# Kernel tuning notes

Hardware: AMD Instinct MI355X
Metric: run time of the kernel (lower is better)

The kernel has to match this reference:

```python
import jax, jax.numpy as jnp
import numpy as np

B, N, C = 4, 2048, 768
H = 12
HD = C // H
SCALE = HD ** -0.5


def setup_inputs() -> dict:
    key = jax.random.key(0)
    k1, k2, k3 = jax.random.split(key, 3)
    x = jax.random.normal(k1, (B, N, C), dtype=jnp.float32)
    w_qkv = jax.random.normal(k2, (3 * C, C), dtype=jnp.float32) * (C ** -0.5)
    w_proj = jax.random.normal(k3, (C, C), dtype=jnp.float32) * (C ** -0.5)
    b_proj = jnp.zeros((C,), dtype=jnp.float32)
    return {"x": x, "w_qkv": w_qkv, "w_proj": w_proj, "b_proj": b_proj}


def reference(x, w_qkv, w_proj, b_proj):
    Bx, Nx, Cx = x.shape
    # qkv linear: x @ W^T -> [B, N, 3C], then split into heads
    qkv = jnp.einsum('bnc,dc->bnd', x, w_qkv)
    qkv = qkv.reshape(Bx, Nx, 3, H, HD).transpose(2, 0, 3, 1, 4)  # [3, B, H, N, HD]
    q, k, v = qkv[0], qkv[1], qkv[2]
    attn = jnp.einsum('bhqd,bhkd->bhqk', q, k) * SCALE  # [B, H, N, N]
    attn = jax.nn.softmax(attn, axis=-1)
    out = jnp.einsum('bhqk,bhkd->bhqd', attn, v)  # [B, H, N, HD]
    out = out.transpose(0, 2, 1, 3).reshape(Bx, Nx, Cx)
    out = jnp.einsum('bnc,dc->bnd', out, w_proj) + b_proj
    return out
```

## Files before the change

### kernel.cpp

```cpp
#include <hip/hip_runtime.h>
#include <hip/hip_bf16.h>
#include <stdint.h>

#define DI __device__ __forceinline__

typedef __bf16 bf16x8 __attribute__((ext_vector_type(8)));
typedef float f32x4 __attribute__((ext_vector_type(4)));
typedef unsigned short u16;

DI u16 f2bf(float f) {
  union { float f; uint32_t u; } x; x.f = f;
  uint32_t r = (x.u + 0x7FFFu + ((x.u >> 16) & 1u)) >> 16;
  return (u16)r;
}
DI bf16x8 load16(const u16* p) { return *(const bf16x8*)p; }

DI void async_copy16(void* lds, const void* g) {
  __builtin_amdgcn_global_load_lds(
      (const __attribute__((address_space(1))) uint32_t*)g,
      (__attribute__((address_space(3))) uint32_t*)lds, 16, 0, 0);
}

DI f32x4 mfma16(bf16x8 a, bf16x8 b, f32x4 c) {
  return __builtin_amdgcn_mfma_f32_16x16x32_bf16(a, b, c, 0, 0, 0);
}

DI uint32_t pk_bf16(float a, float b) {
  union { __hip_bfloat162 v; uint32_t u; } r;
  r.v = __float22bfloat162_rn(make_float2(a, b));
  return r.u;
}

#define QSCALE (0.125f * 1.44269504088896340736f)

__global__ __launch_bounds__(256)
void cvt_all(const float* __restrict__ s0, u16* __restrict__ d0, int n0,
             const float* __restrict__ s1, u16* __restrict__ d1, int n1,
             const float* __restrict__ s2, u16* __restrict__ d2, int n2) {
  int i = (blockIdx.x * 256 + threadIdx.x) * 4;
  const float* s; u16* d;
  if (i < n0) { s = s0 + i; d = d0 + i; }
  else if (i < n0 + n1) { s = s1 + (i - n0); d = d1 + (i - n0); }
  else if (i < n0 + n1 + n2) { s = s2 + (i - n0 - n1); d = d2 + (i - n0 - n1); }
  else return;
  float4 v = *(const float4*)s;
  ushort4 o;
  o.x = f2bf(v.x); o.y = f2bf(v.y); o.z = f2bf(v.z); o.w = f2bf(v.w);
  *(ushort4*)d = o;
}

__global__ __launch_bounds__(256)
void gemm_qkv(const u16* __restrict__ A, const u16* __restrict__ Bm,
              u16* __restrict__ Qb, u16* __restrict__ Kb, u16* __restrict__ Vt,
              int M, int N, int K) {
  __shared__ u16 As[2][128 * 32];
  __shared__ u16 Bs[2][128 * 32];

  const int tid  = threadIdx.x;
  const int lane = tid & 63;
  const int wave = tid >> 6;
  const int lb  = blockIdx.x + 18 * blockIdx.y;
  const int swz = (lb & 7) * 144 + (lb >> 3);
  const int n0 = (swz % 18) * 128;
  const int m0 = (swz / 18) * 128;
  const int wm = (wave & 1) * 64;
  const int wn = (wave >> 1) * 64;
  const int c = lane & 15;
  const int g = lane >> 4;

  f32x4 acc[4][4] = {};

#pragma unroll
  for (int i = 0; i < 2; ++i) {
    int j = i * 256 + tid;
    int row = j >> 2;
    int col = (j & 3) * 8;
    async_copy16(&As[0][j * 8], &A[(size_t)(m0 + row) * K + col]);
    async_copy16(&Bs[0][j * 8], &Bm[(size_t)(n0 + row) * K + col]);
  }

  int cur = 0;
  for (int k0 = 0; k0 < K; k0 += 32) {
    __syncthreads();

    if (k0 + 32 < K) {
#pragma unroll
      for (int i = 0; i < 2; ++i) {
        int j = i * 256 + tid;
        int row = j >> 2;
        int col = (j & 3) * 8;
        async_copy16(&As[cur ^ 1][j * 8],
                     &A[(size_t)(m0 + row) * K + k0 + 32 + col]);
        async_copy16(&Bs[cur ^ 1][j * 8],
                     &Bm[(size_t)(n0 + row) * K + k0 + 32 + col]);
      }
    }

    bf16x8 af[4], bfr[4];
#pragma unroll
    for (int t = 0; t < 4; ++t) {
      af[t]  = *(const bf16x8*)&As[cur][(wm + t * 16 + c) * 32 + g * 8];
      bfr[t] = *(const bf16x8*)&Bs[cur][(wn + t * 16 + c) * 32 + g * 8];
    }
#pragma unroll
    for (int mt = 0; mt < 4; ++mt)
#pragma unroll
      for (int nt = 0; nt < 4; ++nt)
        acc[mt][nt] = mfma16(af[mt], bfr[nt], acc[mt][nt]);
    cur ^= 1;
  }

  if (n0 < 768) {
#pragma unroll
    for (int nt = 0; nt < 4; ++nt) {
      int col = n0 + wn + nt * 16 + c;
#pragma unroll
      for (int mt = 0; mt < 4; ++mt)
#pragma unroll
        for (int r = 0; r < 4; ++r) {
          int row = m0 + wm + mt * 16 + g * 4 + r;
          Qb[(size_t)row * 768 + col] = f2bf(acc[mt][nt][r] * QSCALE);
        }
    }
  } else if (n0 < 1536) {
#pragma unroll
    for (int nt = 0; nt < 4; ++nt) {
      int col = n0 - 768 + wn + nt * 16 + c;
#pragma unroll
      for (int mt = 0; mt < 4; ++mt)
#pragma unroll
        for (int r = 0; r < 4; ++r) {
          int row = m0 + wm + mt * 16 + g * 4 + r;
          Kb[(size_t)row * 768 + col] = f2bf(acc[mt][nt][r]);
        }
    }
  } else {
#pragma unroll
    for (int nt = 0; nt < 4; ++nt) {
      int cv = n0 - 1536 + wn + nt * 16 + c;
      int hv = cv >> 6, d = cv & 63;
#pragma unroll
      for (int mt = 0; mt < 4; ++mt) {
        int row = m0 + wm + mt * 16 + g * 4;
        int b = row >> 11, nn = row & 2047;
        ushort4 o;
        o.x = f2bf(acc[mt][nt][0]); o.y = f2bf(acc[mt][nt][1]);
        o.z = f2bf(acc[mt][nt][2]); o.w = f2bf(acc[mt][nt][3]);
        *(ushort4*)&Vt[(((size_t)b * 12 + hv) * 64 + d) * 2048 + nn] = o;
      }
    }
  }
}

__global__ __launch_bounds__(256)
void gemm_proj(const u16* __restrict__ A, const u16* __restrict__ Bm,
               const float* __restrict__ bias, float* __restrict__ Co,
               int M, int N, int K) {
  __shared__ u16 As[2][128 * 32];
  __shared__ u16 Bs[2][64 * 32];

  const int tid  = threadIdx.x;
  const int lane = tid & 63;
  const int wave = tid >> 6;
  const int lb  = blockIdx.x + 12 * blockIdx.y;
  const int swz = (lb & 7) * 96 + (lb >> 3);
  const int n0 = (swz % 12) * 64;
  const int m0 = (swz / 12) * 128;
  const int wm = (wave & 1) * 64;
  const int wn = (wave >> 1) * 32;
  const int c = lane & 15;
  const int g = lane >> 4;

  f32x4 acc[4][2] = {};

#pragma unroll
  for (int i = 0; i < 2; ++i) {
    int j = i * 256 + tid;
    int row = j >> 2;
    int col = (j & 3) * 8;
    async_copy16(&As[0][j * 8], &A[(size_t)(m0 + row) * K + col]);
  }
  {
    int row = tid >> 2;
    int col = (tid & 3) * 8;
    async_copy16(&Bs[0][tid * 8], &Bm[(size_t)(n0 + row) * K + col]);
  }

  int cur = 0;
  for (int k0 = 0; k0 < K; k0 += 32) {
    __syncthreads();

    if (k0 + 32 < K) {
#pragma unroll
      for (int i = 0; i < 2; ++i) {
        int j = i * 256 + tid;
        int row = j >> 2;
        int col = (j & 3) * 8;
        async_copy16(&As[cur ^ 1][j * 8],
                     &A[(size_t)(m0 + row) * K + k0 + 32 + col]);
      }
      {
        int row = tid >> 2;
        int col = (tid & 3) * 8;
        async_copy16(&Bs[cur ^ 1][tid * 8],
                     &Bm[(size_t)(n0 + row) * K + k0 + 32 + col]);
      }
    }

    bf16x8 af[4], bfr[2];
#pragma unroll
    for (int t = 0; t < 4; ++t)
      af[t] = *(const bf16x8*)&As[cur][(wm + t * 16 + c) * 32 + g * 8];
#pragma unroll
    for (int t = 0; t < 2; ++t)
      bfr[t] = *(const bf16x8*)&Bs[cur][(wn + t * 16 + c) * 32 + g * 8];
#pragma unroll
    for (int mt = 0; mt < 4; ++mt)
#pragma unroll
      for (int nt = 0; nt < 2; ++nt)
        acc[mt][nt] = mfma16(af[mt], bfr[nt], acc[mt][nt]);
    cur ^= 1;
  }

#pragma unroll
  for (int nt = 0; nt < 2; ++nt) {
    int col = n0 + wn + nt * 16 + c;
    float bv = bias[col];
#pragma unroll
    for (int mt = 0; mt < 4; ++mt)
#pragma unroll
      for (int r = 0; r < 4; ++r) {
        int row = m0 + wm + mt * 16 + g * 4 + r;
        Co[(size_t)row * N + col] = acc[mt][nt][r] + bv;
      }
  }
}

__global__ __launch_bounds__(256)
void attn_flash(const u16* __restrict__ Qb, const u16* __restrict__ Kb,
                const u16* __restrict__ Vt, u16* __restrict__ out) {
  __shared__ u16 Ks[2][2 * 64 * 32];
  __shared__ u16 Vs[2][2 * 64 * 32];
  __shared__ __align__(16) u16 Plds[4][32 * 72];

  const int tid  = threadIdx.x;
  const int lane = tid & 63;
  const int wave = tid >> 6;
  const int idx = blockIdx.x;
  const int qchunk = idx & 15;
  const int h = (idx >> 4) % 12;
  const int b = idx / (16 * 12);
  const int q0 = qchunk * 128 + wave * 32;
  const int c = lane & 15;
  const int g = lane >> 4;

  const u16* Qp = Qb + (size_t)b * 2048 * 768 + h * 64;
  const u16* Kp = Kb + (size_t)b * 2048 * 768 + h * 64;
  const u16* Vp = Vt + ((size_t)b * 12 + h) * 64 * 2048;

  u16* pw = &Plds[wave][0];

  const bf16x8 qf0 = load16(&Qp[(size_t)(q0 + c) * 768 + g * 8]);
  const bf16x8 qf1 = load16(&Qp[(size_t)(q0 + c) * 768 + 32 + g * 8]);
  const bf16x8 qg0 = load16(&Qp[(size_t)(q0 + 16 + c) * 768 + g * 8]);
  const bf16x8 qg1 = load16(&Qp[(size_t)(q0 + 16 + c) * 768 + 32 + g * 8]);

  const int kk = tid >> 2;
  const int ch = (tid & 3) * 8;

  float lsum0 = 0.f, lsum1 = 0.f;
  f32x4 o0[4] = {}, o1[4] = {};

  async_copy16(&Ks[0][tid * 8],        &Kp[(size_t)kk * 768 + ch]);
  async_copy16(&Ks[0][2048 + tid * 8], &Kp[(size_t)kk * 768 + 32 + ch]);
  async_copy16(&Vs[0][tid * 8],        &Vp[(size_t)kk * 2048 + ch]);
  async_copy16(&Vs[0][2048 + tid * 8], &Vp[(size_t)kk * 2048 + 32 + ch]);

  int cur = 0;
  for (int k0 = 0; k0 < 2048; k0 += 64) {
    __syncthreads();

    if (k0 + 64 < 2048) {
      int nxt = cur ^ 1, kn = k0 + 64;
      async_copy16(&Ks[nxt][tid * 8],        &Kp[(size_t)(kn + kk) * 768 + ch]);
      async_copy16(&Ks[nxt][2048 + tid * 8], &Kp[(size_t)(kn + kk) * 768 + 32 + ch]);
      async_copy16(&Vs[nxt][tid * 8],        &Vp[(size_t)kk * 2048 + kn + ch]);
      async_copy16(&Vs[nxt][2048 + tid * 8], &Vp[(size_t)kk * 2048 + kn + 32 + ch]);
    }

    f32x4 s0[4] = {}, s1[4] = {};
#pragma unroll
    for (int kt = 0; kt < 4; ++kt) {
      bf16x8 kf0 = *(const bf16x8*)&Ks[cur][(kt * 16 + c) * 32 + g * 8];
      bf16x8 kf1 = *(const bf16x8*)&Ks[cur][2048 + (kt * 16 + c) * 32 + g * 8];
      s0[kt] = mfma16(kf0, qf0, s0[kt]);
      s0[kt] = mfma16(kf1, qf1, s0[kt]);
      s1[kt] = mfma16(kf0, qg0, s1[kt]);
      s1[kt] = mfma16(kf1, qg1, s1[kt]);
    }

#pragma unroll
    for (int kt = 0; kt < 4; ++kt) {
      float p0 = __builtin_amdgcn_exp2f(s0[kt][0]);
      float p1 = __builtin_amdgcn_exp2f(s0[kt][1]);
      float p2 = __builtin_amdgcn_exp2f(s0[kt][2]);
      float p3 = __builtin_amdgcn_exp2f(s0[kt][3]);
      lsum0 += (p0 + p1) + (p2 + p3);
      uint2 w; w.x = pk_bf16(p0, p1); w.y = pk_bf16(p2, p3);
      *(uint2*)&pw[c * 72 + kt * 16 + g * 4] = w;

      float r0 = __builtin_amdgcn_exp2f(s1[kt][0]);
      float r1 = __builtin_amdgcn_exp2f(s1[kt][1]);
      float r2 = __builtin_amdgcn_exp2f(s1[kt][2]);
      float r3 = __builtin_amdgcn_exp2f(s1[kt][3]);
      lsum1 += (r0 + r1) + (r2 + r3);
      uint2 w2; w2.x = pk_bf16(r0, r1); w2.y = pk_bf16(r2, r3);
      *(uint2*)&pw[(16 + c) * 72 + kt * 16 + g * 4] = w2;
    }
    __asm__ volatile("s_waitcnt lgkmcnt(0)" ::: "memory");

#pragma unroll
    for (int kt2 = 0; kt2 < 2; ++kt2) {
      const bf16x8 pf0 = *(const bf16x8*)&pw[c * 72 + kt2 * 32 + g * 8];
      const bf16x8 pf1 = *(const bf16x8*)&pw[(16 + c) * 72 + kt2 * 32 + g * 8];
#pragma unroll
      for (int dt = 0; dt < 4; ++dt) {
        bf16x8 vf = *(const bf16x8*)&Vs[cur][kt2 * 2048 + (dt * 16 + c) * 32 + g * 8];
        o0[dt] = mfma16(pf0, vf, o0[dt]);
        o1[dt] = mfma16(pf1, vf, o1[dt]);
      }
    }
    cur ^= 1;
  }

  float t0 = lsum0 + __shfl_xor(lsum0, 16);
  t0 += __shfl_xor(t0, 32);
  float t1 = lsum1 + __shfl_xor(lsum1, 16);
  t1 += __shfl_xor(t1, 32);
  float inv0 = 1.f / t0;
  float inv1 = 1.f / t1;
  float invr0[4], invr1[4];
#pragma unroll
  for (int r = 0; r < 4; ++r) {
    invr0[r] = __shfl(inv0, g * 4 + r);
    invr1[r] = __shfl(inv1, g * 4 + r);
  }

#pragma unroll
  for (int dt = 0; dt < 4; ++dt)
#pragma unroll
    for (int r = 0; r < 4; ++r) {
      int n = q0 + g * 4 + r;
      out[(size_t)(b * 2048 + n) * 768 + h * 64 + dt * 16 + c] =
          f2bf(o0[dt][r] * invr0[r]);
      out[(size_t)(b * 2048 + n + 16) * 768 + h * 64 + dt * 16 + c] =
          f2bf(o1[dt][r] * invr1[r]);
    }
}

extern "C" void kernel_launch(void* const* d_in, const int* in_sizes, int n_in,
                              void* d_out, int out_size, void* d_ws, size_t ws_size,
                              hipStream_t stream) {
  const float* x      = (const float*)d_in[0];
  const float* w_qkv  = (const float*)d_in[1];
  const float* w_proj = (const float*)d_in[2];
  const float* b_proj = (const float*)d_in[3];
  float* out = (float*)d_out;

  const int M = 8192;
  const int C = 768;
  const int NQKV = 2304;

  u16* xb     = (u16*)d_ws;
  u16* wqkvb  = xb + (size_t)M * C;
  u16* wprojb = wqkvb + (size_t)NQKV * C;
  u16* Qb     = wprojb + (size_t)C * C;
  u16* Kb     = Qb + (size_t)M * C;
  u16* Vt     = Kb + (size_t)M * C;
  u16* attn   = Vt + (size_t)M * C;

  dim3 blk(256);
  const int n0 = M * C, n1 = NQKV * C, n2 = C * C;
  cvt_all<<<dim3((n0 + n1 + n2) / 1024), blk, 0, stream>>>(
      x, xb, n0, w_qkv, wqkvb, n1, w_proj, wprojb, n2);

  gemm_qkv<<<dim3(NQKV / 128, M / 128), blk, 0, stream>>>(
      xb, wqkvb, Qb, Kb, Vt, M, NQKV, C);
  attn_flash<<<dim3(4 * 12 * 16), blk, 0, stream>>>(Qb, Kb, Vt, attn);
  gemm_proj<<<dim3(C / 64, M / 128), blk, 0, stream>>>(
      attn, wprojb, b_proj, out, M, C, C);
}
```

Before: 221.2 us.

## Enlarge QKV GEMM tile to 256x128 with 512 threads and swizzle attention blocks

The QKV projection GEMM now uses 512-thread blocks that each compute a 256x128 output tile. Each of the 8 waves owns a 128x32 sub-tile, and the grid shrinks to 576 blocks. The attention kernel's block index is remapped with an XCD-style swizzle so blocks sharing the same batch and head land together, aiming for better L2 reuse of K and V. The wave shape changes to 8x2 MFMA tiles per k-step, which loads more A fragments per wave and may raise register pressure.

```diff
diff --git a/kernel.cpp b/kernel.cpp
--- a/kernel.cpp
+++ b/kernel.cpp
@@ -49,34 +49,36 @@
   *(ushort4*)d = o;
 }
 
-__global__ __launch_bounds__(256)
+__global__ __launch_bounds__(512)
 void gemm_qkv(const u16* __restrict__ A, const u16* __restrict__ Bm,
               u16* __restrict__ Qb, u16* __restrict__ Kb, u16* __restrict__ Vt,
               int M, int N, int K) {
-  __shared__ u16 As[2][128 * 32];
+  __shared__ u16 As[2][256 * 32];
   __shared__ u16 Bs[2][128 * 32];
 
   const int tid  = threadIdx.x;
   const int lane = tid & 63;
   const int wave = tid >> 6;
   const int lb  = blockIdx.x + 18 * blockIdx.y;
-  const int swz = (lb & 7) * 144 + (lb >> 3);
+  const int swz = (lb & 7) * 72 + (lb >> 3);
   const int n0 = (swz % 18) * 128;
-  const int m0 = (swz / 18) * 128;
-  const int wm = (wave & 1) * 64;
-  const int wn = (wave >> 1) * 64;
+  const int m0 = (swz / 18) * 256;
+  const int wm = (wave & 1) * 128;
+  const int wn = (wave >> 1) * 32;
   const int c = lane & 15;
   const int g = lane >> 4;
 
-  f32x4 acc[4][4] = {};
+  f32x4 acc[8][2] = {};
 
 #pragma unroll
   for (int i = 0; i < 2; ++i) {
-    int j = i * 256 + tid;
-    int row = j >> 2;
-    int col = (j & 3) * 8;
+    int j = i * 512 + tid;
+    int row = j >> 2, col = (j & 3) * 8;
     async_copy16(&As[0][j * 8], &A[(size_t)(m0 + row) * K + col]);
-    async_copy16(&Bs[0][j * 8], &Bm[(size_t)(n0 + row) * K + col]);
+  }
+  {
+    int row = tid >> 2, col = (tid & 3) * 8;
+    async_copy16(&Bs[0][tid * 8], &Bm[(size_t)(n0 + row) * K + col]);
   }
 
   int cur = 0;
@@ -86,36 +88,39 @@
     if (k0 + 32 < K) {
 #pragma unroll
       for (int i = 0; i < 2; ++i) {
-        int j = i * 256 + tid;
-        int row = j >> 2;
-        int col = (j & 3) * 8;
+        int j = i * 512 + tid;
+        int row = j >> 2, col = (j & 3) * 8;
         async_copy16(&As[cur ^ 1][j * 8],
                      &A[(size_t)(m0 + row) * K + k0 + 32 + col]);
-        async_copy16(&Bs[cur ^ 1][j * 8],
+      }
+      {
+        int row = tid >> 2, col = (tid & 3) * 8;
+        async_copy16(&Bs[cur ^ 1][tid * 8],
                      &Bm[(size_t)(n0 + row) * K + k0 + 32 + col]);
       }
     }
 
-    bf16x8 af[4], bfr[4];
-#pragma unroll
-    for (int t = 0; t < 4; ++t) {
-      af[t]  = *(const bf16x8*)&As[cur][(wm + t * 16 + c) * 32 + g * 8];
+    bf16x8 af[8], bfr[2];
+#pragma unroll
+    for (int t = 0; t < 8; ++t)
+      af[t] = *(const bf16x8*)&As[cur][(wm + t * 16 + c) * 32 + g * 8];
+#pragma unroll
+    for (int t = 0; t < 2; ++t)
       bfr[t] = *(const bf16x8*)&Bs[cur][(wn + t * 16 + c) * 32 + g * 8];
-    }
-#pragma unroll
-    for (int mt = 0; mt < 4; ++mt)
-#pragma unroll
-      for (int nt = 0; nt < 4; ++nt)
+#pragma unroll
+    for (int mt = 0; mt < 8; ++mt)
+#pragma unroll
+      for (int nt = 0; nt < 2; ++nt)
         acc[mt][nt] = mfma16(af[mt], bfr[nt], acc[mt][nt]);
     cur ^= 1;
   }
 
   if (n0 < 768) {
 #pragma unroll
-    for (int nt = 0; nt < 4; ++nt) {
+    for (int nt = 0; nt < 2; ++nt) {
       int col = n0 + wn + nt * 16 + c;
 #pragma unroll
-      for (int mt = 0; mt < 4; ++mt)
+      for (int mt = 0; mt < 8; ++mt)
 #pragma unroll
         for (int r = 0; r < 4; ++r) {
           int row = m0 + wm + mt * 16 + g * 4 + r;
@@ -124,10 +129,10 @@
     }
   } else if (n0 < 1536) {
 #pragma unroll
-    for (int nt = 0; nt < 4; ++nt) {
+    for (int nt = 0; nt < 2; ++nt) {
       int col = n0 - 768 + wn + nt * 16 + c;
 #pragma unroll
-      for (int mt = 0; mt < 4; ++mt)
+      for (int mt = 0; mt < 8; ++mt)
 #pragma unroll
         for (int r = 0; r < 4; ++r) {
           int row = m0 + wm + mt * 16 + g * 4 + r;
@@ -136,11 +141,11 @@
     }
   } else {
 #pragma unroll
-    for (int nt = 0; nt < 4; ++nt) {
+    for (int nt = 0; nt < 2; ++nt) {
       int cv = n0 - 1536 + wn + nt * 16 + c;
       int hv = cv >> 6, d = cv & 63;
 #pragma unroll
-      for (int mt = 0; mt < 4; ++mt) {
+      for (int mt = 0; mt < 8; ++mt) {
         int row = m0 + wm + mt * 16 + g * 4;
         int b = row >> 11, nn = row & 2047;
         ushort4 o;
@@ -176,13 +181,11 @@
 #pragma unroll
   for (int i = 0; i < 2; ++i) {
     int j = i * 256 + tid;
-    int row = j >> 2;
-    int col = (j & 3) * 8;
+    int row = j >> 2, col = (j & 3) * 8;
     async_copy16(&As[0][j * 8], &A[(size_t)(m0 + row) * K + col]);
   }
   {
-    int row = tid >> 2;
-    int col = (tid & 3) * 8;
+    int row = tid >> 2, col = (tid & 3) * 8;
     async_copy16(&Bs[0][tid * 8], &Bm[(size_t)(n0 + row) * K + col]);
   }
 
@@ -194,14 +197,12 @@
 #pragma unroll
       for (int i = 0; i < 2; ++i) {
         int j = i * 256 + tid;
-        int row = j >> 2;
-        int col = (j & 3) * 8;
+        int row = j >> 2, col = (j & 3) * 8;
         async_copy16(&As[cur ^ 1][j * 8],
                      &A[(size_t)(m0 + row) * K + k0 + 32 + col]);
       }
       {
-        int row = tid >> 2;
-        int col = (tid & 3) * 8;
+        int row = tid >> 2, col = (tid & 3) * 8;
         async_copy16(&Bs[cur ^ 1][tid * 8],
                      &Bm[(size_t)(n0 + row) * K + k0 + 32 + col]);
       }
@@ -246,10 +247,11 @@
   const int tid  = threadIdx.x;
   const int lane = tid & 63;
   const int wave = tid >> 6;
-  const int idx = blockIdx.x;
-  const int qchunk = idx & 15;
-  const int h = (idx >> 4) % 12;
-  const int b = idx / (16 * 12);
+  const int bid = blockIdx.x;
+  const int swz = (bid & 7) * 96 + (bid >> 3);
+  const int qchunk = swz & 15;
+  const int h = (swz >> 4) % 12;
+  const int b = swz / 192;
   const int q0 = qchunk * 128 + wave * 32;
   const int c = lane & 15;
   const int g = lane >> 4;
@@ -384,7 +386,7 @@
   cvt_all<<<dim3((n0 + n1 + n2) / 1024), blk, 0, stream>>>(
       x, xb, n0, w_qkv, wqkvb, n1, w_proj, wprojb, n2);
 
-  gemm_qkv<<<dim3(NQKV / 128, M / 128), blk, 0, stream>>>(
+  gemm_qkv<<<dim3(NQKV / 128, M / 256), dim3(512), 0, stream>>>(
       xb, wqkvb, Qb, Kb, Vt, M, NQKV, C);
   attn_flash<<<dim3(4 * 12 * 16), blk, 0, stream>>>(Qb, Kb, Vt, attn);
   gemm_proj<<<dim3(C / 64, M / 128), blk, 0, stream>>>(
```

After: 225.1 us. About the same (+1.8%).
